# Optimization experiments

Measured on AMD Instinct MI355X. Metric: run time of the kernel, lower is better.

## Reference

```python
import jax, jax.numpy as jnp
import numpy as np

# Production-scale sampled 2-hop GraphSAGE flow
N, C, HID, OUT = 1_000_000, 128, 32, 16
NSRC1, NDST1, E1 = 600_000, 80_000, 1_280_000
NDST2, E2 = 8_000, 80_000


def setup_inputs() -> dict:
    key = jax.random.key(0)
    ks = jax.random.split(key, 8)
    x = jax.random.normal(ks[0], (N, C), jnp.float32)
    n_id = jax.random.randint(ks[1], (NSRC1,), 0, N)
    src1 = jax.random.randint(ks[2], (E1,), 0, NSRC1)
    dst1 = jax.random.randint(ks[3], (E1,), 0, NDST1)
    src2 = jax.random.randint(ks[4], (E2,), 0, NDST1)
    dst2 = jax.random.randint(ks[5], (E2,), 0, NDST2)
    W1 = jax.random.normal(ks[6], (C, HID), jnp.float32) / np.sqrt(C).astype(np.float32)
    b1 = jnp.zeros((HID,), jnp.float32)
    W2 = jax.random.normal(ks[7], (HID, OUT), jnp.float32) / np.sqrt(HID).astype(np.float32)
    b2 = jnp.zeros((OUT,), jnp.float32)
    return dict(x=x, n_id=n_id, src1=src1, dst1=dst1, src2=src2, dst2=dst2,
                W1=W1, b1=b1, W2=W2, b2=b2)


def _mean_agg(feat_src, src, dst, num_dst):
    # scatter-mean of source features onto destination nodes (PyG aggr='mean')
    msg = feat_src[src]                                          # [E, F]
    s = jax.ops.segment_sum(msg, dst, num_segments=num_dst)      # [num_dst, F]
    cnt = jax.ops.segment_sum(jnp.ones((src.shape[0],), feat_src.dtype), dst,
                              num_segments=num_dst)
    return s / jnp.maximum(cnt, 1.0)[:, None]


def reference(x, n_id, src1, dst1, src2, dst2, W1, b1, W2, b2):
    h = x[n_id]                                  # gather sampled nodes [NSRC1, C]
    # SAGEConv(concat=False, normalize=False): mean-agg then linear
    h = _mean_agg(h, src1, dst1, NDST1) @ W1 + b1
    h = jax.nn.relu(h)                           # F.dropout(p=0.5) is a no-op in eval
    h = _mean_agg(h, src2, dst2, NDST2) @ W2 + b2
    return jax.nn.log_softmax(h, axis=1)
```

## Files before the change

kernel.cpp:

```cpp
#include <hip/hip_runtime.h>
#include <hip/hip_fp16.h>
#include <math.h>

#define N_NODES  1000000
#define C_IN     128
#define HID      32
#define OUTF     16
#define NSRC1    600000
#define NDST1    80000
#define E1       1280000
#define NDST2    8000
#define E2       80000

#define KB1 4688
#define HB1 5000
#define HB2 313
#define AB1 313
#define AB2 32

#define T1A  1250
#define T1B  (KB1 - T1A)
#define GRP2 1719

typedef _Float16 f16x8 __attribute__((ext_vector_type(8)));
typedef float    f32x4 __attribute__((ext_vector_type(4)));

__device__ __forceinline__ void transform_body(
    const float* __restrict__ x, const int* __restrict__ n_id,
    const float* __restrict__ W1, __half* __restrict__ p,
    _Float16* W1f , int idx)
{
    for (int i = threadIdx.x; i < 4096; i += 256) {
        int j  = i & 7;
        int ln = (i >> 3) & 63;
        int h  = (i >> 9) & 1;
        int s  = i >> 10;
        int k  = 32 * s + ((ln >> 4) << 3) + j;
        int c  = (h << 4) + (ln & 15);
        W1f[i] = (_Float16)W1[k * HID + c];
    }
    __syncthreads();

    const int wave = threadIdx.x >> 6;
    const int lane = threadIdx.x & 63;
    const int gwave = idx * 4 + wave;
    if (gwave >= NSRC1 / 32) return;
    const int s0 = gwave * 32;

    const int r15 = lane & 15;
    const int q   = lane >> 4;

    const float* xrow0 = x + (size_t)n_id[s0 + r15]      * C_IN + q * 8;
    const float* xrow1 = x + (size_t)n_id[s0 + 16 + r15] * C_IN + q * 8;

    float4 xf[2][4][2];
    #pragma unroll
    for (int s = 0; s < 4; ++s) {
        xf[0][s][0] = *(const float4*)(xrow0 + 32 * s);
        xf[0][s][1] = *(const float4*)(xrow0 + 32 * s + 4);
        xf[1][s][0] = *(const float4*)(xrow1 + 32 * s);
        xf[1][s][1] = *(const float4*)(xrow1 + 32 * s + 4);
    }

    f16x8 wf[4][2];
    #pragma unroll
    for (int s = 0; s < 4; ++s)
        #pragma unroll
        for (int h = 0; h < 2; ++h)
            wf[s][h] = *((const f16x8*)W1f + ((s * 2 + h) * 64 + lane));

    f32x4 acc[2][2];
    #pragma unroll
    for (int mt = 0; mt < 2; ++mt)
        #pragma unroll
        for (int h = 0; h < 2; ++h)
            acc[mt][h] = (f32x4){0.f, 0.f, 0.f, 0.f};

    #pragma unroll
    for (int mt = 0; mt < 2; ++mt) {
        #pragma unroll
        for (int s = 0; s < 4; ++s) {
            f16x8 bf;
            float4 lo = xf[mt][s][0], hi = xf[mt][s][1];
            bf[0] = (_Float16)lo.x; bf[1] = (_Float16)lo.y;
            bf[2] = (_Float16)lo.z; bf[3] = (_Float16)lo.w;
            bf[4] = (_Float16)hi.x; bf[5] = (_Float16)hi.y;
            bf[6] = (_Float16)hi.z; bf[7] = (_Float16)hi.w;
            #pragma unroll
            for (int h = 0; h < 2; ++h)
                acc[mt][h] = __builtin_amdgcn_mfma_f32_16x16x32_f16(
                    wf[s][h], bf, acc[mt][h], 0, 0, 0);
        }
    }

    #pragma unroll
    for (int mt = 0; mt < 2; ++mt) {
        #pragma unroll
        for (int h = 0; h < 2; ++h) {
            union { __half2 v[2]; uint2 u; } pk;
            pk.v[0] = __floats2half2_rn(acc[mt][h][0], acc[mt][h][1]);
            pk.v[1] = __floats2half2_rn(acc[mt][h][2], acc[mt][h][3]);
            *(uint2*)&p[(size_t)(s0 + mt * 16 + r15) * HID + h * 16 + q * 4] = pk.u;
        }
    }
}

__global__ __launch_bounds__(256) void kA1_hist_transform(
    const float* __restrict__ x, const int* __restrict__ n_id,
    const float* __restrict__ W1, __half* __restrict__ p,
    const int* __restrict__ dst1, const int* __restrict__ dst2,
    int* __restrict__ deg1, int* __restrict__ deg2)
{
    __shared__ _Float16 W1f[4096];

    const int bid = blockIdx.x;
    const int t = bid / 5, r = bid % 5;
    if (r == 0 && t < T1A) {
        transform_body(x, n_id, W1, p, W1f, t);
        return;
    }
    const int nt = min((bid + 4) / 5, T1A);
    const int h  = bid - nt;
    if (h < HB1) {
        int e = h * 256 + threadIdx.x;
        if (e < E1) atomicAdd(&deg1[dst1[e]], 1);
    } else {
        int e = (h - HB1) * 256 + threadIdx.x;
        if (e < E2) atomicAdd(&deg2[dst2[e]], 1);
    }
}

__global__ __launch_bounds__(256) void kB_alloc(
    const int* __restrict__ deg1, const int* __restrict__ deg2,
    int* __restrict__ rs1, int* __restrict__ rs2,
    int* __restrict__ cur1, int* __restrict__ cur2,
    int* __restrict__ counters)
{
    const int bid  = blockIdx.x;
    const int lane = threadIdx.x & 63;
    const int* deg; int* rs; int* cur; int* ctr; int nd; int d;
    if (bid < AB1) { deg = deg1; rs = rs1; cur = cur1; ctr = counters + 0;
                     nd = NDST1; d = bid * 256 + threadIdx.x; }
    else           { deg = deg2; rs = rs2; cur = cur2; ctr = counters + 1;
                     nd = NDST2; d = (bid - AB1) * 256 + threadIdx.x; }

    int v = (d < nd) ? deg[d] : 0;
    int incl = v;
    #pragma unroll
    for (int off = 1; off < 64; off <<= 1) {
        int t = __shfl_up(incl, off, 64);
        if (lane >= off) incl += t;
    }
    int total = __shfl(incl, 63, 64);
    int base = 0;
    if (lane == 63) base = atomicAdd(ctr, total);
    base = __shfl(base, 63, 64);
    if (d < nd) { int r = base + incl - v; rs[d] = r; cur[d] = r; }
}

__global__ __launch_bounds__(256) void kA2_bucket_transform(
    const float* __restrict__ x, const int* __restrict__ n_id,
    const float* __restrict__ W1, __half* __restrict__ p,
    const int* __restrict__ src1, const int* __restrict__ dst1,
    const int* __restrict__ src2, const int* __restrict__ dst2,
    int* __restrict__ cur1, int* __restrict__ cur2,
    int* __restrict__ ss1, int* __restrict__ ss2)
{
    __shared__ _Float16 W1f[4096];

    const int bid = blockIdx.x;
    const int g = bid / 5, r = bid % 5;
    int bidx;
    if (g < GRP2) {
        if (r < 2) {
            int ti = 2 * g + r;
            if (ti < T1B) {
                transform_body(x, n_id, W1, p, W1f, T1A + ti);
                return;
            }
            bidx = 0;
        } else {
            bidx = 3 * g + (r - 2);
        }
    } else {
        bidx = 3 * GRP2 + (bid - 5 * GRP2);
    }

    if (bidx < HB1) {
        int e = bidx * 256 + threadIdx.x;
        if (e < E1) {
            int d = dst1[e];
            int pos = atomicAdd(&cur1[d], 1);
            ss1[pos] = src1[e];
        }
    } else {
        int e = (bidx - HB1) * 256 + threadIdx.x;
        if (e < E2) {
            int d = dst2[e];
            int pos = atomicAdd(&cur2[d], 1);
            ss2[pos] = src2[e];
        }
    }
}

__global__ __launch_bounds__(256) void kD_gather1(
    const int* __restrict__ row_start, const int* __restrict__ deg,
    const int* __restrict__ ss1, const __half* __restrict__ p,
    const float* __restrict__ b1, const float* __restrict__ W2,
    float* __restrict__ q)
{
    __shared__ float hbuf[16][HID + 1];
    const int g = threadIdx.x >> 4;
    const int f = threadIdx.x & 15;
    const int d = blockIdx.x * 16 + g;

    float w2r[HID];
    #pragma unroll
    for (int k = 0; k < HID; ++k) w2r[k] = W2[k * OUTF + f];
    const float2 b1v = *(const float2*)&b1[2 * f];

    const int start = row_start[d];
    const int dg    = deg[d];
    const __half2* ph2 = (const __half2*)p;

    float2 acc = make_float2(0.f, 0.f);
    int i = 0;
    for (; i + 4 <= dg; i += 4) {
        int s0 = ss1[start + i];
        int s1 = ss1[start + i + 1];
        int s2 = ss1[start + i + 2];
        int s3 = ss1[start + i + 3];
        float2 a = __half22float2(ph2[(size_t)s0 * 16 + f]);
        float2 b = __half22float2(ph2[(size_t)s1 * 16 + f]);
        float2 c = __half22float2(ph2[(size_t)s2 * 16 + f]);
        float2 e = __half22float2(ph2[(size_t)s3 * 16 + f]);
        acc.x += (a.x + b.x) + (c.x + e.x);
        acc.y += (a.y + b.y) + (c.y + e.y);
    }
    for (; i < dg; ++i) {
        float2 a = __half22float2(ph2[(size_t)ss1[start + i] * 16 + f]);
        acc.x += a.x; acc.y += a.y;
    }

    const float inv = 1.f / (float)max(dg, 1);
    hbuf[g][2 * f]     = fmaxf(acc.x * inv + b1v.x, 0.f);
    hbuf[g][2 * f + 1] = fmaxf(acc.y * inv + b1v.y, 0.f);
    float o = 0.f;
    #pragma unroll
    for (int k = 0; k < HID; ++k) o += hbuf[g][k] * w2r[k];
    q[(size_t)d * OUTF + f] = o;
}

__global__ __launch_bounds__(256) void kE_gather2_lsm(
    const int* __restrict__ row_start2, const int* __restrict__ deg2,
    const int* __restrict__ ss2, const float* __restrict__ q,
    const float* __restrict__ b2, float* __restrict__ out)
{
    const int g = threadIdx.x >> 4;
    const int f = threadIdx.x & 15;
    const int d = blockIdx.x * 16 + g;
    if (d >= NDST2) return;

    const int start = row_start2[d];
    const int dg    = deg2[d];

    float acc = 0.f;
    int i = 0;
    for (; i + 2 <= dg; i += 2) {
        int s0 = ss2[start + i];
        int s1 = ss2[start + i + 1];
        acc += q[(size_t)s0 * OUTF + f] + q[(size_t)s1 * OUTF + f];
    }
    if (i < dg) acc += q[(size_t)ss2[start + i] * OUTF + f];

    float z = acc / (float)max(dg, 1) + b2[f];
    float m = z;
    #pragma unroll
    for (int off = 8; off; off >>= 1) m = fmaxf(m, __shfl_xor(m, off, 16));
    float e = expf(z - m);
    float s = e;
    #pragma unroll
    for (int off = 8; off; off >>= 1) s += __shfl_xor(s, off, 16);
    out[(size_t)d * OUTF + f] = z - m - logf(s);
}

extern "C" void kernel_launch(void* const* d_in, const int* in_sizes, int n_in,
                              void* d_out, int out_size, void* d_ws, size_t ws_size,
                              hipStream_t stream)
{
    const float* x    = (const float*)d_in[0];
    const int*   n_id = (const int*)  d_in[1];
    const int*   src1 = (const int*)  d_in[2];
    const int*   dst1 = (const int*)  d_in[3];
    const int*   src2 = (const int*)  d_in[4];
    const int*   dst2 = (const int*)  d_in[5];
    const float* W1   = (const float*)d_in[6];
    const float* b1   = (const float*)d_in[7];
    const float* W2   = (const float*)d_in[8];
    const float* b2   = (const float*)d_in[9];
    float* out = (float*)d_out;

    char* ws = (char*)d_ws;
    __half* p       = (__half*)(ws + 0);
    int*   ss1      = (int*)   (ws + 38400000);
    int*   ss2      = (int*)   (ws + 43520000);
    int*   deg1     = (int*)   (ws + 43840000);
    int*   deg2     = (int*)   (ws + 44160000);
    int*   counters = (int*)   (ws + 44192000);
    int*   rs1      = (int*)   (ws + 44192064);
    int*   rs2      = (int*)   (ws + 44512064);
    int*   cur1     = (int*)   (ws + 44544064);
    int*   cur2     = (int*)   (ws + 44864064);
    float* q        = (float*) (ws + 44896064);

    hipMemsetAsync(deg1, 0, 352064, stream);

    kA1_hist_transform<<<T1A + HB1 + HB2, 256, 0, stream>>>(
        x, n_id, W1, p, dst1, dst2, deg1, deg2);

    kB_alloc<<<AB1 + AB2, 256, 0, stream>>>(deg1, deg2, rs1, rs2, cur1, cur2,
                                            counters);

    kA2_bucket_transform<<<T1B + HB1 + HB2, 256, 0, stream>>>(
        x, n_id, W1, p, src1, dst1, src2, dst2, cur1, cur2, ss1, ss2);

    kD_gather1<<<NDST1 / 16, 256, 0, stream>>>(rs1, deg1, ss1, p, b1, W2, q);

    kE_gather2_lsm<<<NDST2 / 16, 256, 0, stream>>>(rs2, deg2, ss2, q, b2, out);
}
```

Before: 748.5 us.

## Widen layer-1 gather to 16-byte loads and rebalance transform interleave

The first-hop gather kernel now gives each destination 4 lanes instead of 16. Each lane loads 16 bytes (eight halves) per neighbour, and neighbour indices are shared between lanes with wave shuffles. Each block covers 64 destinations and then runs the W2 projection in four passes. This cuts the number of memory instructions per edge. Separately, the transform blocks are split evenly between the histogram and bucketing kernels with a 1-in-3 interleave, replacing the uneven 1250/3438 split. The trade-offs are more per-thread registers and fewer threads per destination, which can hurt latency hiding on high-degree rows.

```diff
diff --git a/kernel.cpp b/kernel.cpp
--- a/kernel.cpp
+++ b/kernel.cpp
@@ -18,9 +18,8 @@
 #define AB1 313
 #define AB2 32
 
-#define T1A  1250
+#define T1A  2344
 #define T1B  (KB1 - T1A)
-#define GRP2 1719
 
 typedef _Float16 f16x8 __attribute__((ext_vector_type(8)));
 typedef float    f32x4 __attribute__((ext_vector_type(4)));
@@ -114,12 +113,11 @@
     __shared__ _Float16 W1f[4096];
 
     const int bid = blockIdx.x;
-    const int t = bid / 5, r = bid % 5;
-    if (r == 0 && t < T1A) {
-        transform_body(x, n_id, W1, p, W1f, t);
+    if ((bid % 3) == 0 && (bid / 3) < T1A) {
+        transform_body(x, n_id, W1, p, W1f, bid / 3);
         return;
     }
-    const int nt = min((bid + 4) / 5, T1A);
+    const int nt = min(bid / 3 + 1, T1A);
     const int h  = bid - nt;
     if (h < HB1) {
         int e = h * 256 + threadIdx.x;
@@ -169,22 +167,12 @@
     __shared__ _Float16 W1f[4096];
 
     const int bid = blockIdx.x;
-    const int g = bid / 5, r = bid % 5;
-    int bidx;
-    if (g < GRP2) {
-        if (r < 2) {
-            int ti = 2 * g + r;
-            if (ti < T1B) {
-                transform_body(x, n_id, W1, p, W1f, T1A + ti);
-                return;
-            }
-            bidx = 0;
-        } else {
-            bidx = 3 * g + (r - 2);
-        }
-    } else {
-        bidx = 3 * GRP2 + (bid - 5 * GRP2);
-    }
+    if ((bid % 3) == 0 && (bid / 3) < T1B) {
+        transform_body(x, n_id, W1, p, W1f, T1A + bid / 3);
+        return;
+    }
+    const int nt   = min(bid / 3 + 1, T1B);
+    const int bidx = bid - nt;
 
     if (bidx < HB1) {
         int e = bidx * 256 + threadIdx.x;
@@ -209,46 +197,81 @@
     const float* __restrict__ b1, const float* __restrict__ W2,
     float* __restrict__ q)
 {
-    __shared__ float hbuf[16][HID + 1];
-    const int g = threadIdx.x >> 4;
+    __shared__ float hbuf[64][HID + 1];
+    const int lane = threadIdx.x & 63;
+    const int g  = threadIdx.x >> 2;
+    const int f4 = threadIdx.x & 3;
+    const int d0 = blockIdx.x * 64;
+    const int d  = d0 + g;
+
     const int f = threadIdx.x & 15;
-    const int d = blockIdx.x * 16 + g;
-
     float w2r[HID];
     #pragma unroll
     for (int k = 0; k < HID; ++k) w2r[k] = W2[k * OUTF + f];
-    const float2 b1v = *(const float2*)&b1[2 * f];
+
+    const float4 b1v0 = *(const float4*)&b1[f4 * 8];
+    const float4 b1v1 = *(const float4*)&b1[f4 * 8 + 4];
 
     const int start = row_start[d];
     const int dg    = deg[d];
-    const __half2* ph2 = (const __half2*)p;
-
-    float2 acc = make_float2(0.f, 0.f);
+    const float4* p4 = (const float4*)p;
+
+    float acc[8];
+    #pragma unroll
+    for (int j = 0; j < 8; ++j) acc[j] = 0.f;
+
+    const int base = lane & ~3;
     int i = 0;
     for (; i + 4 <= dg; i += 4) {
-        int s0 = ss1[start + i];
-        int s1 = ss1[start + i + 1];
-        int s2 = ss1[start + i + 2];
-        int s3 = ss1[start + i + 3];
-        float2 a = __half22float2(ph2[(size_t)s0 * 16 + f]);
-        float2 b = __half22float2(ph2[(size_t)s1 * 16 + f]);
-        float2 c = __half22float2(ph2[(size_t)s2 * 16 + f]);
-        float2 e = __half22float2(ph2[(size_t)s3 * 16 + f]);
-        acc.x += (a.x + b.x) + (c.x + e.x);
-        acc.y += (a.y + b.y) + (c.y + e.y);
+        int s_own = ss1[start + i + f4];
+        #pragma unroll
+        for (int j = 0; j < 4; ++j) {
+            int s = __shfl(s_own, base + j, 64);
+            float4 v = p4[(size_t)s * 4 + f4];
+            const __half2* h2 = (const __half2*)&v;
+            float2 t0 = __half22float2(h2[0]);
+            float2 t1 = __half22float2(h2[1]);
+            float2 t2 = __half22float2(h2[2]);
+            float2 t3 = __half22float2(h2[3]);
+            acc[0] += t0.x; acc[1] += t0.y;
+            acc[2] += t1.x; acc[3] += t1.y;
+            acc[4] += t2.x; acc[5] += t2.y;
+            acc[6] += t3.x; acc[7] += t3.y;
+        }
     }
     for (; i < dg; ++i) {
-        float2 a = __half22float2(ph2[(size_t)ss1[start + i] * 16 + f]);
-        acc.x += a.x; acc.y += a.y;
+        int s = ss1[start + i];
+        float4 v = p4[(size_t)s * 4 + f4];
+        const __half2* h2 = (const __half2*)&v;
+        float2 t0 = __half22float2(h2[0]);
+        float2 t1 = __half22float2(h2[1]);
+        float2 t2 = __half22float2(h2[2]);
+        float2 t3 = __half22float2(h2[3]);
+        acc[0] += t0.x; acc[1] += t0.y;
+        acc[2] += t1.x; acc[3] += t1.y;
+        acc[4] += t2.x; acc[5] += t2.y;
+        acc[6] += t3.x; acc[7] += t3.y;
     }
 
     const float inv = 1.f / (float)max(dg, 1);
-    hbuf[g][2 * f]     = fmaxf(acc.x * inv + b1v.x, 0.f);
-    hbuf[g][2 * f + 1] = fmaxf(acc.y * inv + b1v.y, 0.f);
-    float o = 0.f;
-    #pragma unroll
-    for (int k = 0; k < HID; ++k) o += hbuf[g][k] * w2r[k];
-    q[(size_t)d * OUTF + f] = o;
+    hbuf[g][f4 * 8 + 0] = fmaxf(acc[0] * inv + b1v0.x, 0.f);
+    hbuf[g][f4 * 8 + 1] = fmaxf(acc[1] * inv + b1v0.y, 0.f);
+    hbuf[g][f4 * 8 + 2] = fmaxf(acc[2] * inv + b1v0.z, 0.f);
+    hbuf[g][f4 * 8 + 3] = fmaxf(acc[3] * inv + b1v0.w, 0.f);
+    hbuf[g][f4 * 8 + 4] = fmaxf(acc[4] * inv + b1v1.x, 0.f);
+    hbuf[g][f4 * 8 + 5] = fmaxf(acc[5] * inv + b1v1.y, 0.f);
+    hbuf[g][f4 * 8 + 6] = fmaxf(acc[6] * inv + b1v1.z, 0.f);
+    hbuf[g][f4 * 8 + 7] = fmaxf(acc[7] * inv + b1v1.w, 0.f);
+    __syncthreads();
+
+    #pragma unroll
+    for (int pass = 0; pass < 4; ++pass) {
+        const int dl = pass * 16 + (threadIdx.x >> 4);
+        float o = 0.f;
+        #pragma unroll
+        for (int k = 0; k < HID; ++k) o += hbuf[dl][k] * w2r[k];
+        q[(size_t)(d0 + dl) * OUTF + f] = o;
+    }
 }
 
 __global__ __launch_bounds__(256) void kE_gather2_lsm(
@@ -324,7 +347,7 @@
     kA2_bucket_transform<<<T1B + HB1 + HB2, 256, 0, stream>>>(
         x, n_id, W1, p, src1, dst1, src2, dst2, cur1, cur2, ss1, ss2);
 
-    kD_gather1<<<NDST1 / 16, 256, 0, stream>>>(rs1, deg1, ss1, p, b1, W2, q);
+    kD_gather1<<<NDST1 / 64, 256, 0, stream>>>(rs1, deg1, ss1, p, b1, W2, q);
 
     kE_gather2_lsm<<<NDST2 / 16, 256, 0, stream>>>(rs2, deg2, ss2, q, b2, out);
 }
```

New measurement: 743.0 us. Within noise of the previous version (-0.7%).
